# Kernel tuning notes

Measured on AMD Instinct MI355X. Metric: run time of the kernel, lower is better.

The kernel has to match this reference:

```python
import jax, jax.numpy as jnp
import numpy as np

N_G, N_D = 100000, 50000
E_GG, E_DG = 1600000, 800000
IN, HID, H, OUT = 128, 128, 8, 2
D = HID // H  # 16


def setup_inputs() -> dict:
    key = jax.random.key(0)
    ks = jax.random.split(key, 14)
    w = lambda k, s: jax.random.normal(k, s, dtype=jnp.float32) * 0.05
    return {
        "x_gene": jax.random.normal(ks[0], (N_G, IN), dtype=jnp.float32),
        "x_disease": jax.random.normal(ks[1], (N_D, IN), dtype=jnp.float32),
        "edge_gg": jax.random.randint(ks[2], (2, E_GG), 0, N_G),   # gene -> gene
        "edge_dg": jax.random.randint(ks[3], (2, E_DG), 0, N_D),   # disease -> gene (dst < N_D <= N_G)
        "proj_gene_w": w(ks[4], (HID, IN)),
        "proj_gene_b": jnp.zeros((HID,), jnp.float32),
        "proj_disease_w": w(ks[5], (HID, IN)),
        "proj_disease_b": jnp.zeros((HID,), jnp.float32),
        "att_src_gg": w(ks[6], (H, D)),
        "att_dst_gg": w(ks[7], (H, D)),
        "att_src_dg": w(ks[8], (H, D)),
        "att_dst_dg": w(ks[9], (H, D)),
        "k_lin_w": w(ks[10], (HID, HID)),
        "k_lin_b": jnp.zeros((HID,), jnp.float32),
        "q": w(ks[11], (HID,)),
        "lin_w": w(ks[12], (OUT, HID)),
        "lin_b": jnp.zeros((OUT,), jnp.float32),
    }


def _edge_type_out(x_src, x_dst, att_src, att_dst, src, dst, num_dst):
    """GAT-style message passing for one edge type. x_*: [N,H,D]."""
    a_s = (x_src * att_src).sum(-1)          # [Ns, H]
    a_d = (x_dst * att_dst).sum(-1)          # [Nd, H]
    a = a_s[src] + a_d[dst]                  # [E, H]
    a = jnp.where(a > 0, a, 0.2 * a)         # leaky_relu(0.2)
    # segment softmax over edges grouped by dst node
    m = jax.ops.segment_max(a, dst, num_segments=num_dst)
    m = jnp.where(jnp.isfinite(m), m, 0.0)
    e = jnp.exp(a - m[dst])
    s = jax.ops.segment_sum(e, dst, num_segments=num_dst)
    alpha = e / (s[dst] + 1e-16)             # [E, H]
    msg = x_src[src] * alpha[:, :, None]     # [E, H, D]
    out = jax.ops.segment_sum(msg, dst, num_segments=num_dst)
    return jax.nn.relu(out.reshape(num_dst, H * D))


def reference(x_gene, x_disease, edge_gg, edge_dg,
              proj_gene_w, proj_gene_b, proj_disease_w, proj_disease_b,
              att_src_gg, att_dst_gg, att_src_dg, att_dst_dg,
              k_lin_w, k_lin_b, q, lin_w, lin_b):
    # per-node-type projection, split into heads
    xg = (x_gene @ proj_gene_w.T + proj_gene_b).reshape(N_G, H, D)
    xd = (x_disease @ proj_disease_w.T + proj_disease_b).reshape(N_D, H, D)

    # node-level attention per edge type (dropout p=0.6 is train-only; eval mode here)
    out_gg = _edge_type_out(xg, xg, att_src_gg, att_dst_gg, edge_gg[0], edge_gg[1], N_G)
    out_dg = _edge_type_out(xd, xg, att_src_dg, att_dst_dg, edge_dg[0], edge_dg[1], N_G)

    # semantic-level attention across metapaths for dst type 'gene'
    outs = jnp.stack([out_gg, out_dg])                  # [2, N_G, HID]
    k = jnp.tanh(outs @ k_lin_w.T + k_lin_b)            # [2, N_G, HID]
    score = (q * k.mean(axis=1)).sum(-1)                # [2]
    attn = jax.nn.softmax(score, axis=0)
    fused = (attn[:, None, None] * outs).sum(0)         # [N_G, HID]

    return fused @ lin_w.T + lin_b                      # [N_G, OUT]
```

## Files before the change

### kernel.cpp

```cpp
#include <hip/hip_runtime.h>
#include <hip/hip_fp16.h>
#include <math.h>

#define NG 100000
#define ND 50000
#define EGG 1600000
#define EDG 800000
#define EALL (EGG + EDG)
#define NALL (NG + NG)
#define HID 128
#define NH 8

#define SHIFT 11
#define BDSTS (1 << SHIFT)
#define NBUK  ((NALL + BDSTS - 1) / BDSTS)
#define BUKCAP 36864
#define S1_CH 6144
#define KM_HALF ((NG + 127) / 128)

#define OFF_OUT_GG 0UL
#define OFF_OUT_DG 6400000UL
#define OFF_XG     12800000UL
#define OFF_XD     19200000UL
#define OFF_ASG    22400000UL
#define OFF_ADG    23200000UL
#define OFF_ADD    24000000UL
#define OFF_ASD    24800000UL
#define OFF_KPART  25200000UL
#define OFF_BCNT   25200256UL
#define ZERO_BASE  OFF_KPART
#define ZERO_CNT   384
#define OFF_ATTN   25200384UL
#define OFF_BBASE  25200512UL
#define OFF_RP     25200640UL
#define OFF_COL    25400704UL
#define OFF_WTIL   27800704UL
#define OFF_BTIL   27803776UL
#define OFF_WTILD  27803904UL
#define OFF_BTILD  27804928UL

typedef float  f32x4  __attribute__((ext_vector_type(4)));
typedef short  bf16x8 __attribute__((ext_vector_type(8)));
typedef _Float16 f16x8 __attribute__((ext_vector_type(8)));
#define MFMA(a, b, c)  __builtin_amdgcn_mfma_f32_16x16x32_bf16(a, b, c, 0, 0, 0)
#define MFMAH(a, b, c) __builtin_amdgcn_mfma_f32_16x16x32_f16(a, b, c, 0, 0, 0)

#define FMAMIX_LO(ACC, SRC, AL) \
    asm("v_fma_mix_f32 %0, %1, %2, %0 op_sel:[0,0,0] op_sel_hi:[1,0,0]" \
        : "+v"(ACC) : "v"(SRC), "v"(AL))
#define FMAMIX_HI(ACC, SRC, AL) \
    asm("v_fma_mix_f32 %0, %1, %2, %0 op_sel:[1,0,0] op_sel_hi:[1,0,0]" \
        : "+v"(ACC) : "v"(SRC), "v"(AL))

__device__ __forceinline__ unsigned short bf16_rne(float f) {
    unsigned u = __float_as_uint(f);
    u += 0x7FFFu + ((u >> 16) & 1u);
    return (unsigned short)(u >> 16);
}
__device__ __forceinline__ float bf16f(unsigned short h) {
    return __uint_as_float(((unsigned)h) << 16);
}
__device__ __forceinline__ unsigned short f16_bits(float f) {
    __half h = __float2half(f);
    return *(unsigned short*)&h;
}
__device__ __forceinline__ float fast_tanh(float x) {
    x = fminf(fmaxf(x, -15.f), 15.f);
    float t = __expf(2.f * x);
    return (t - 1.f) / (t + 1.f);
}
__device__ __forceinline__ bf16x8 cvt_hi8(f32x4 v0, f32x4 v1) {
    bf16x8 f;
    f[0] = (short)bf16_rne(v0.x); f[1] = (short)bf16_rne(v0.y);
    f[2] = (short)bf16_rne(v0.z); f[3] = (short)bf16_rne(v0.w);
    f[4] = (short)bf16_rne(v1.x); f[5] = (short)bf16_rne(v1.y);
    f[6] = (short)bf16_rne(v1.z); f[7] = (short)bf16_rne(v1.w);
    return f;
}
__device__ __forceinline__ bf16x8 cvt_lo8(f32x4 v0, f32x4 v1, bf16x8 h) {
    bf16x8 f;
    f[0] = (short)bf16_rne(v0.x - bf16f((unsigned short)h[0]));
    f[1] = (short)bf16_rne(v0.y - bf16f((unsigned short)h[1]));
    f[2] = (short)bf16_rne(v0.z - bf16f((unsigned short)h[2]));
    f[3] = (short)bf16_rne(v0.w - bf16f((unsigned short)h[3]));
    f[4] = (short)bf16_rne(v1.x - bf16f((unsigned short)h[4]));
    f[5] = (short)bf16_rne(v1.y - bf16f((unsigned short)h[5]));
    f[6] = (short)bf16_rne(v1.z - bf16f((unsigned short)h[6]));
    f[7] = (short)bf16_rne(v1.w - bf16f((unsigned short)h[7]));
    return f;
}
__device__ __forceinline__ unsigned relu_pk(unsigned u) {
    return u & ~(((u & 0x80008000u) >> 15) * 0xFFFFu);
}
union U4F16 { uint4 u; f16x8 f; };

__global__ void init_zero_k(float* __restrict__ p, int n) {
    int i = blockIdx.x * 256 + threadIdx.x;
    if (i < n) p[i] = 0.f;
}

__global__ void make_wtil(const float* __restrict__ W, const float* __restrict__ bias,
                          const float* __restrict__ a0, const float* __restrict__ a1,
                          const float* __restrict__ a2, int natt,
                          float* __restrict__ wtil, float* __restrict__ btil) {
    int tot = natt * 8 * 128;
    for (int i = blockIdx.x * 256 + threadIdx.x; i < tot; i += gridDim.x * 256) {
        int k = i & 127, cc = i >> 7;
        int v = cc >> 3, h = cc & 7;
        const float* av = (v == 0) ? a0 : (v == 1) ? a1 : a2;
        float s = 0.f;
        #pragma unroll
        for (int c = 0; c < 16; c++) s += av[h * 16 + c] * W[(h * 16 + c) * 128 + k];
        wtil[i] = s;
    }
    if (blockIdx.x == 0 && threadIdx.x < natt * 8) {
        int v = threadIdx.x >> 3, h = threadIdx.x & 7;
        const float* av = (v == 0) ? a0 : (v == 1) ? a1 : a2;
        float s = 0.f;
        #pragma unroll
        for (int c = 0; c < 16; c++) s += av[h * 16 + c] * bias[h * 16 + c];
        btil[threadIdx.x] = s;
    }
}

template<int NATT>
__launch_bounds__(256)
__global__ void proj_mfma(const float* __restrict__ x, const float* __restrict__ W,
                          const float* __restrict__ bias,
                          const float* __restrict__ wtil, const float* __restrict__ btil,
                          unsigned short* __restrict__ xbf,
                          float* __restrict__ o0, float* __restrict__ o1,
                          float* __restrict__ o2, int N) {
    constexpr int NTE = (NATT * 8 + 15) / 16;
    constexpr int NT = 8 + NTE;
    __shared__ bf16x8 Bhi[NT * 4 * 64];
    __shared__ bf16x8 Blo[8 * 4 * 64];
    for (int idx = threadIdx.x; idx < 128 * 32; idx += 256) {
        int row = idx >> 5, kq = idx & 31;
        f32x4 v = *(const f32x4*)&W[row * 128 + kq * 4];
        int ct = row >> 4, c = row & 15;
        int k0 = kq * 4;
        int kc = k0 >> 5, q16 = (k0 & 31) >> 3, j2 = (k0 & 7) >> 1;
        int slot = (ct * 4 + kc) * 64 + q16 * 16 + c;
        unsigned short hx = bf16_rne(v.x), hy = bf16_rne(v.y);
        unsigned short hz = bf16_rne(v.z), hw = bf16_rne(v.w);
        unsigned* dh = (unsigned*)&Bhi[slot];
        dh[j2]     = ((unsigned)hy << 16) | hx;
        dh[j2 + 1] = ((unsigned)hw << 16) | hz;
        unsigned* dl = (unsigned*)&Blo[slot];
        dl[j2]     = ((unsigned)bf16_rne(v.y - bf16f(hy)) << 16) | bf16_rne(v.x - bf16f(hx));
        dl[j2 + 1] = ((unsigned)bf16_rne(v.w - bf16f(hw)) << 16) | bf16_rne(v.z - bf16f(hz));
    }
    for (int idx = threadIdx.x; idx < NTE * 16 * 32; idx += 256) {
        int cc = idx >> 5, kq = idx & 31;
        f32x4 v = {0.f, 0.f, 0.f, 0.f};
        if (cc < NATT * 8) v = *(const f32x4*)&wtil[cc * 128 + kq * 4];
        int ct = 8 + (cc >> 4), c = cc & 15;
        int k0 = kq * 4;
        int kc = k0 >> 5, q16 = (k0 & 31) >> 3, j2 = (k0 & 7) >> 1;
        unsigned* dh = (unsigned*)&Bhi[(ct * 4 + kc) * 64 + q16 * 16 + c];
        dh[j2]     = ((unsigned)bf16_rne(v.y) << 16) | bf16_rne(v.x);
        dh[j2 + 1] = ((unsigned)bf16_rne(v.w) << 16) | bf16_rne(v.z);
    }
    __syncthreads();
    int wv = threadIdx.x >> 6, l = threadIdx.x & 63;
    int q = l >> 4, c16 = l & 15;
    int rw = blockIdx.x * 128 + wv * 32;
    int n0 = min(rw + c16, N - 1);
    int n1 = min(rw + 16 + c16, N - 1);
    const float* xr0 = &x[(size_t)n0 * 128 + q * 8];
    const float* xr1 = &x[(size_t)n1 * 128 + q * 8];
    #define LOADX(FH, FL, PTR, OFF) \
        bf16x8 FH, FL; \
        { f32x4 v0_ = *(const f32x4*)((PTR) + (OFF)); \
          f32x4 v1_ = *(const f32x4*)((PTR) + (OFF) + 4); \
          FH = cvt_hi8(v0_, v1_); FL = cvt_lo8(v0_, v1_, FH); }
    LOADX(xh00, xl00, xr0, 0)  LOADX(xh01, xl01, xr0, 32)
    LOADX(xh02, xl02, xr0, 64) LOADX(xh03, xl03, xr0, 96)
    LOADX(xh10, xl10, xr1, 0)  LOADX(xh11, xl11, xr1, 32)
    LOADX(xh12, xl12, xr1, 64) LOADX(xh13, xl13, xr1, 96)
    #undef LOADX
    int r0 = rw + q * 4;
    int r1 = r0 + 16;
    #define CT_MAIN(CT) { \
        bf16x8 bh0 = Bhi[((CT) * 4 + 0) * 64 + l]; \
        bf16x8 bh1 = Bhi[((CT) * 4 + 1) * 64 + l]; \
        bf16x8 bh2 = Bhi[((CT) * 4 + 2) * 64 + l]; \
        bf16x8 bh3 = Bhi[((CT) * 4 + 3) * 64 + l]; \
        bf16x8 bl0 = Blo[((CT) * 4 + 0) * 64 + l]; \
        bf16x8 bl1 = Blo[((CT) * 4 + 1) * 64 + l]; \
        bf16x8 bl2 = Blo[((CT) * 4 + 2) * 64 + l]; \
        bf16x8 bl3 = Blo[((CT) * 4 + 3) * 64 + l]; \
        f32x4 aA = {0,0,0,0}, aB = {0,0,0,0}, aC = {0,0,0,0}, aD = {0,0,0,0}; \
        aA = MFMA(xh00, bh0, aA); aB = MFMA(xh01, bh1, aB); \
        aC = MFMA(xh10, bh0, aC); aD = MFMA(xh11, bh1, aD); \
        aA = MFMA(xl00, bh0, aA); aB = MFMA(xl01, bh1, aB); \
        aC = MFMA(xl10, bh0, aC); aD = MFMA(xl11, bh1, aD); \
        aA = MFMA(xh00, bl0, aA); aB = MFMA(xh01, bl1, aB); \
        aC = MFMA(xh10, bl0, aC); aD = MFMA(xh11, bl1, aD); \
        aA = MFMA(xh02, bh2, aA); aB = MFMA(xh03, bh3, aB); \
        aC = MFMA(xh12, bh2, aC); aD = MFMA(xh13, bh3, aD); \
        aA = MFMA(xl02, bh2, aA); aB = MFMA(xl03, bh3, aB); \
        aC = MFMA(xl12, bh2, aC); aD = MFMA(xl13, bh3, aD); \
        aA = MFMA(xh02, bl2, aA); aB = MFMA(xh03, bl3, aB); \
        aC = MFMA(xh12, bl2, aC); aD = MFMA(xh13, bl3, aD); \
        f32x4 d0 = aA + aB, d1 = aC + aD; \
        float bv = bias[(CT) * 16 + c16]; \
        int col = (CT) * 16 + c16; \
        if (r0 + 0 < N) xbf[(size_t)(r0 + 0) * 128 + col] = f16_bits(d0[0] + bv); \
        if (r0 + 1 < N) xbf[(size_t)(r0 + 1) * 128 + col] = f16_bits(d0[1] + bv); \
        if (r0 + 2 < N) xbf[(size_t)(r0 + 2) * 128 + col] = f16_bits(d0[2] + bv); \
        if (r0 + 3 < N) xbf[(size_t)(r0 + 3) * 128 + col] = f16_bits(d0[3] + bv); \
        if (r1 + 0 < N) xbf[(size_t)(r1 + 0) * 128 + col] = f16_bits(d1[0] + bv); \
        if (r1 + 1 < N) xbf[(size_t)(r1 + 1) * 128 + col] = f16_bits(d1[1] + bv); \
        if (r1 + 2 < N) xbf[(size_t)(r1 + 2) * 128 + col] = f16_bits(d1[2] + bv); \
        if (r1 + 3 < N) xbf[(size_t)(r1 + 3) * 128 + col] = f16_bits(d1[3] + bv); }
    CT_MAIN(0) CT_MAIN(1) CT_MAIN(2) CT_MAIN(3)
    CT_MAIN(4) CT_MAIN(5) CT_MAIN(6) CT_MAIN(7)
    #undef CT_MAIN
    #define CT_ATT(TE) { \
        bf16x8 bh0 = Bhi[((8 + (TE)) * 4 + 0) * 64 + l]; \
        bf16x8 bh1 = Bhi[((8 + (TE)) * 4 + 1) * 64 + l]; \
        bf16x8 bh2 = Bhi[((8 + (TE)) * 4 + 2) * 64 + l]; \
        bf16x8 bh3 = Bhi[((8 + (TE)) * 4 + 3) * 64 + l]; \
        f32x4 aA = {0,0,0,0}, aB = {0,0,0,0}, aC = {0,0,0,0}, aD = {0,0,0,0}; \
        aA = MFMA(xh00, bh0, aA); aB = MFMA(xh01, bh1, aB); \
        aC = MFMA(xh10, bh0, aC); aD = MFMA(xh11, bh1, aD); \
        aA = MFMA(xh02, bh2, aA); aB = MFMA(xh03, bh3, aB); \
        aC = MFMA(xh12, bh2, aC); aD = MFMA(xh13, bh3, aD); \
        f32x4 d0 = aA + aB, d1 = aC + aD; \
        int cc = (TE) * 16 + c16; \
        if (cc < NATT * 8) { \
            float bt = btil[cc]; \
            int v = cc >> 3, h = cc & 7; \
            float* op = (v == 0) ? o0 : ((v == 1) ? o1 : o2); \
            if (r0 + 0 < N) op[(r0 + 0) * 8 + h] = d0[0] + bt; \
            if (r0 + 1 < N) op[(r0 + 1) * 8 + h] = d0[1] + bt; \
            if (r0 + 2 < N) op[(r0 + 2) * 8 + h] = d0[2] + bt; \
            if (r0 + 3 < N) op[(r0 + 3) * 8 + h] = d0[3] + bt; \
            if (r1 + 0 < N) op[(r1 + 0) * 8 + h] = d1[0] + bt; \
            if (r1 + 1 < N) op[(r1 + 1) * 8 + h] = d1[1] + bt; \
            if (r1 + 2 < N) op[(r1 + 2) * 8 + h] = d1[2] + bt; \
            if (r1 + 3 < N) op[(r1 + 3) * 8 + h] = d1[3] + bt; } }
    CT_ATT(0)
    if constexpr (NTE > 1) { CT_ATT(1) }
    #undef CT_ATT
}

__launch_bounds__(256)
__global__ void fused_scatter(const int* __restrict__ gg_src, const int* __restrict__ gg_dst,
                              const int* __restrict__ dg_src, const int* __restrict__ dg_dst,
                              int* __restrict__ bcnt, unsigned int* __restrict__ colPacked) {
    __shared__ int cnt[256], scanE[256], gbase[256], cursor[256];
    __shared__ int ss[256];
    __shared__ unsigned int sorted[S1_CH];
    __shared__ unsigned char bof[S1_CH];
    int t = threadIdx.x;
    cnt[t] = 0;
    __syncthreads();
    int base = blockIdx.x * S1_CH;
    for (int k = 0; k < S1_CH; k += 256) {
        int e = base + k + t;
        if (e < EALL) {
            int dn = (e < EGG) ? gg_dst[e] : (NG + dg_dst[e - EGG]);
            atomicAdd(&cnt[dn >> SHIFT], 1);
        }
    }
    __syncthreads();
    int v = cnt[t];
    ss[t] = v;
    __syncthreads();
    for (int off = 1; off < 256; off <<= 1) {
        int y = (t >= off) ? ss[t - off] : 0;
        __syncthreads();
        ss[t] += y;
        __syncthreads();
    }
    scanE[t] = ss[t] - v;
    cursor[t] = ss[t] - v;
    if (t < NBUK && v > 0) gbase[t] = atomicAdd(&bcnt[t], v);
    __syncthreads();
    for (int k = 0; k < S1_CH; k += 256) {
        int e = base + k + t;
        if (e < EALL) {
            int s, dn;
            if (e < EGG) { s = gg_src[e]; dn = gg_dst[e]; }
            else         { s = dg_src[e - EGG]; dn = NG + dg_dst[e - EGG]; }
            int b = dn >> SHIFT;
            int slot = atomicAdd(&cursor[b], 1);
            sorted[slot] = ((unsigned int)s << SHIFT) | (unsigned int)(dn & (BDSTS - 1));
            bof[slot] = (unsigned char)b;
        }
    }
    __syncthreads();
    int total = ss[255];
    for (int f = t; f < total; f += 256) {
        int b = bof[f];
        colPacked[(size_t)b * BUKCAP + gbase[b] + (f - scanE[b])] = sorted[f];
    }
}

__global__ void scan_buckets(const int* __restrict__ bcnt, int* __restrict__ bbase,
                             int* __restrict__ rp) {
    __shared__ int s[128];
    int t = threadIdx.x;
    int v = (t < NBUK) ? bcnt[t] : 0;
    s[t] = v;
    __syncthreads();
    for (int off = 1; off < 128; off <<= 1) {
        int y = (t >= off) ? s[t - off] : 0;
        __syncthreads();
        s[t] += y;
        __syncthreads();
    }
    if (t < NBUK) bbase[t] = s[t] - v;
    if (t == 0) rp[NALL] = EALL;
}

__launch_bounds__(256)
__global__ void bucket_build(const unsigned int* __restrict__ colPacked,
                             const int* __restrict__ bcnt, const int* __restrict__ bbase,
                             int* __restrict__ rp, int* __restrict__ col) {
    __shared__ int lcur[BDSTS];
    __shared__ int tsum[256];
    int b = blockIdx.x;
    int t = threadIdx.x;
    int d0 = b << SHIFT;
    int nd = min(BDSTS, NALL - d0);
    int cnt = bcnt[b];
    const unsigned int* pk = colPacked + (size_t)b * BUKCAP;
    for (int i = t; i < BDSTS; i += 256) lcur[i] = 0;
    __syncthreads();
    for (int i = t; i < cnt; i += 256)
        atomicAdd(&lcur[pk[i] & (BDSTS - 1)], 1);
    __syncthreads();
    int h0 = lcur[t * 8 + 0], h1 = lcur[t * 8 + 1], h2 = lcur[t * 8 + 2], h3 = lcur[t * 8 + 3];
    int h4 = lcur[t * 8 + 4], h5 = lcur[t * 8 + 5], h6 = lcur[t * 8 + 6], h7 = lcur[t * 8 + 7];
    int tot = h0 + h1 + h2 + h3 + h4 + h5 + h6 + h7;
    tsum[t] = tot;
    __syncthreads();
    for (int off = 1; off < 256; off <<= 1) {
        int y = (t >= off) ? tsum[t - off] : 0;
        __syncthreads();
        tsum[t] += y;
        __syncthreads();
    }
    int gb = bbase[b];
    int pp = tsum[t] - tot + gb;
    __syncthreads();
    #define EMIT(J, HJ) { int idx = t * 8 + (J); \
        if (idx < nd) rp[d0 + idx] = pp; \
        lcur[idx] = pp; pp += (HJ); }
    EMIT(0, h0) EMIT(1, h1) EMIT(2, h2) EMIT(3, h3)
    EMIT(4, h4) EMIT(5, h5) EMIT(6, h6) EMIT(7, h7)
    #undef EMIT
    __syncthreads();
    for (int i = t; i < cnt; i += 256) {
        unsigned int p = pk[i];
        int pos = atomicAdd(&lcur[p & (BDSTS - 1)], 1);
        col[pos] = (int)(p >> SHIFT);
    }
}

__launch_bounds__(256)
__global__ void gat_gather_all(const int* __restrict__ rp, const int* __restrict__ col,
                               const float* __restrict__ as_gg, const float* __restrict__ ad_gg,
                               const unsigned short* __restrict__ xg_h,
                               const float* __restrict__ as_dg, const float* __restrict__ ad_dg,
                               const unsigned short* __restrict__ xd_h,
                               unsigned short* __restrict__ out_gg,
                               unsigned short* __restrict__ out_dg) {
    int wid = (blockIdx.x * 256 + threadIdx.x) >> 6;
    int l = threadIdx.x & 63;
    if (wid >= NALL) return;
    int isdg = wid >= NG;
    int d = isdg ? wid - NG : wid;
    const float* a_s = isdg ? as_dg : as_gg;
    const float* a_d = isdg ? ad_dg : ad_gg;
    const unsigned short* xbf = isdg ? xd_h : xg_h;
    unsigned short* outh = (isdg ? out_dg : out_gg);

    int base = rp[wid];
    int deg = rp[wid + 1] - base;

    int hl = l & 7;
    int g  = l >> 3;
    float adl = a_d[d * 8 + hl];
    float ssum = 0.f;
    for (int c0 = 0; c0 < deg; c0 += 64) {
        int myi = c0 + l;
        int colreg = (myi < deg) ? col[base + myi] : 0;
        int lim = min(deg - c0, 64);
        for (int t = g; t < lim; t += 8) {
            int s = __shfl(colreg, t);
            float a = a_s[s * 8 + hl] + adl;
            a = a > 0.f ? a : 0.2f * a;
            ssum += __expf(a);
        }
    }
    ssum += __shfl_xor(ssum, 8);
    ssum += __shfl_xor(ssum, 16);
    ssum += __shfl_xor(ssum, 32);
    float rsc = 1.f / (ssum + 1e-16f);

    int q = l >> 4;
    int cq = l & 15;
    int hq = cq >> 1;
    uint32_t colbyte = (uint32_t)cq << 4;
    float a0 = 0.f, a1 = 0.f, a2 = 0.f, a3 = 0.f, a4 = 0.f, a5 = 0.f, a6 = 0.f, a7 = 0.f;
    for (int c0 = 0; c0 < deg; c0 += 64) {
        int myi = c0 + l;
        int colreg = (myi < deg) ? col[base + myi] : 0;
        int lim = min(deg - c0, 64);
        for (int j8 = 0; j8 < lim; j8 += 8) {
            float alpha;
            {
                int s = __shfl(colreg, j8 + g);
                float a = a_s[s * 8 + hl] + adl;
                a = a > 0.f ? a : 0.2f * a;
                alpha = __expf(a) * rsc;
            }
            int jlim = min(lim - j8, 8);
            #pragma unroll
            for (int sub = 0; sub < 8; sub += 4) {
                int jrel = sub + q;
                int s = __shfl(colreg, j8 + jrel);
                float al = __shfl(alpha, (jrel << 3) + hq);
                al = (jrel < jlim) ? al : 0.f;
                const uint4 rv = *(const uint4*)((const char*)xbf +
                                    (((size_t)(uint32_t)s << 8) + colbyte));
                FMAMIX_LO(a0, rv.x, al); FMAMIX_HI(a1, rv.x, al);
                FMAMIX_LO(a2, rv.y, al); FMAMIX_HI(a3, rv.y, al);
                FMAMIX_LO(a4, rv.z, al); FMAMIX_HI(a5, rv.z, al);
                FMAMIX_LO(a6, rv.w, al); FMAMIX_HI(a7, rv.w, al);
            }
        }
    }
    a0 += __shfl_xor(a0, 16); a0 += __shfl_xor(a0, 32);
    a1 += __shfl_xor(a1, 16); a1 += __shfl_xor(a1, 32);
    a2 += __shfl_xor(a2, 16); a2 += __shfl_xor(a2, 32);
    a3 += __shfl_xor(a3, 16); a3 += __shfl_xor(a3, 32);
    a4 += __shfl_xor(a4, 16); a4 += __shfl_xor(a4, 32);
    a5 += __shfl_xor(a5, 16); a5 += __shfl_xor(a5, 32);
    a6 += __shfl_xor(a6, 16); a6 += __shfl_xor(a6, 32);
    a7 += __shfl_xor(a7, 16); a7 += __shfl_xor(a7, 32);
    if (q == 0) {
        __half2 h01 = __floats2half2_rn(a0, a1);
        __half2 h23 = __floats2half2_rn(a2, a3);
        __half2 h45 = __floats2half2_rn(a4, a5);
        __half2 h67 = __floats2half2_rn(a6, a7);
        uint4 o;
        o.x = *(unsigned*)&h01; o.y = *(unsigned*)&h23;
        o.z = *(unsigned*)&h45; o.w = *(unsigned*)&h67;
        *(uint4*)((char*)outh + (size_t)d * 256 + cq * 16) = o;
    }
}

__launch_bounds__(256)
__global__ void kmean_mfma(const unsigned short* __restrict__ srcA,
                           const unsigned short* __restrict__ srcB,
                           const float* __restrict__ W, const float* __restrict__ bias,
                           float* __restrict__ kp) {
    __shared__ f16x8 Bs[8 * 4 * 64];
    for (int idx = threadIdx.x; idx < 128 * 32; idx += 256) {
        int row = idx >> 5, kq = idx & 31;
        f32x4 v = *(const f32x4*)&W[row * 128 + kq * 4];
        int ct = row >> 4, c = row & 15;
        int k0 = kq * 4;
        int kc = k0 >> 5, q16 = (k0 & 31) >> 3, j2 = (k0 & 7) >> 1;
        unsigned* dst = (unsigned*)&Bs[(ct * 4 + kc) * 64 + q16 * 16 + c];
        dst[j2]     = ((unsigned)f16_bits(v.y) << 16) | f16_bits(v.x);
        dst[j2 + 1] = ((unsigned)f16_bits(v.w) << 16) | f16_bits(v.z);
    }
    __syncthreads();
    int half = blockIdx.x >= KM_HALF;
    const unsigned short* src = half ? srcB : srcA;
    float* kpp = half ? (kp + 128) : kp;
    int rb = (half ? blockIdx.x - KM_HALF : blockIdx.x) * 128;
    int wv = threadIdx.x >> 6, l = threadIdx.x & 63;
    int q = l >> 4, c16 = l & 15;
    int rw = rb + wv * 32;
    const char* xr0 = (const char*)src + (size_t)(rw + c16) * 256 + q * 16;
    const char* xr1 = xr0 + 16 * 256;
    #define LOADA(F, PTR, OFF) f16x8 F; { \
        U4F16 u_; u_.u = *(const uint4*)((PTR) + (OFF)); \
        u_.u.x = relu_pk(u_.u.x); u_.u.y = relu_pk(u_.u.y); \
        u_.u.z = relu_pk(u_.u.z); u_.u.w = relu_pk(u_.u.w); \
        F = u_.f; }
    LOADA(f00, xr0, 0) LOADA(f01, xr0, 64) LOADA(f02, xr0, 128) LOADA(f03, xr0, 192)
    LOADA(f10, xr1, 0) LOADA(f11, xr1, 64) LOADA(f12, xr1, 128) LOADA(f13, xr1, 192)
    #undef LOADA
    float bv0 = bias[c16],      bv1 = bias[16 + c16], bv2 = bias[32 + c16], bv3 = bias[48 + c16];
    float bv4 = bias[64 + c16], bv5 = bias[80 + c16], bv6 = bias[96 + c16], bv7 = bias[112 + c16];
    int row0 = rw + q * 4;
    int row1 = row0 + 16;
    float cs0 = 0.f, cs1 = 0.f, cs2 = 0.f, cs3 = 0.f, cs4 = 0.f, cs5 = 0.f, cs6 = 0.f, cs7 = 0.f;
    #define CT_STEP(CT, CS, BV) { \
        f16x8 b0 = Bs[((CT) * 4 + 0) * 64 + l]; \
        f16x8 b1 = Bs[((CT) * 4 + 1) * 64 + l]; \
        f16x8 b2 = Bs[((CT) * 4 + 2) * 64 + l]; \
        f16x8 b3 = Bs[((CT) * 4 + 3) * 64 + l]; \
        f32x4 aA = {0,0,0,0}, aB = {0,0,0,0}, aC = {0,0,0,0}, aD = {0,0,0,0}; \
        aA = MFMAH(f00, b0, aA); aB = MFMAH(f01, b1, aB); \
        aA = MFMAH(f02, b2, aA); aB = MFMAH(f03, b3, aB); \
        aC = MFMAH(f10, b0, aC); aD = MFMAH(f11, b1, aD); \
        aC = MFMAH(f12, b2, aC); aD = MFMAH(f13, b3, aD); \
        f32x4 d0 = aA + aB, d1 = aC + aD; \
        float s = 0.f; \
        if (row0 + 0 < NG) s += fast_tanh(d0[0] + (BV)); \
        if (row0 + 1 < NG) s += fast_tanh(d0[1] + (BV)); \
        if (row0 + 2 < NG) s += fast_tanh(d0[2] + (BV)); \
        if (row0 + 3 < NG) s += fast_tanh(d0[3] + (BV)); \
        if (row1 + 0 < NG) s += fast_tanh(d1[0] + (BV)); \
        if (row1 + 1 < NG) s += fast_tanh(d1[1] + (BV)); \
        if (row1 + 2 < NG) s += fast_tanh(d1[2] + (BV)); \
        if (row1 + 3 < NG) s += fast_tanh(d1[3] + (BV)); \
        CS += s; }
    CT_STEP(0, cs0, bv0) CT_STEP(1, cs1, bv1) CT_STEP(2, cs2, bv2) CT_STEP(3, cs3, bv3)
    CT_STEP(4, cs4, bv4) CT_STEP(5, cs5, bv5) CT_STEP(6, cs6, bv6) CT_STEP(7, cs7, bv7)
    #undef CT_STEP
    __syncthreads();
    float* red = (float*)Bs;
    #define REDUCE_CT(CT, CS) { \
        float v = (CS); \
        v += __shfl_xor(v, 16); v += __shfl_xor(v, 32); \
        if (l < 16) red[wv * 128 + (CT) * 16 + l] = v; }
    REDUCE_CT(0, cs0) REDUCE_CT(1, cs1) REDUCE_CT(2, cs2) REDUCE_CT(3, cs3)
    REDUCE_CT(4, cs4) REDUCE_CT(5, cs5) REDUCE_CT(6, cs6) REDUCE_CT(7, cs7)
    #undef REDUCE_CT
    __syncthreads();
    if (threadIdx.x < 128) {
        float s = red[threadIdx.x] + red[128 + threadIdx.x]
                + red[256 + threadIdx.x] + red[384 + threadIdx.x];
        atomicAdd(&kpp[threadIdx.x], s);
    }
}

__global__ void score_attn(const float* __restrict__ kpart, const float* __restrict__ q,
                           float* __restrict__ attn) {
    __shared__ float r0[128], r1[128];
    int t = threadIdx.x;
    r0[t] = q[t] * kpart[t];
    r1[t] = q[t] * kpart[128 + t];
    __syncthreads();
    for (int s = 64; s > 0; s >>= 1) {
        if (t < s) { r0[t] += r0[t + s]; r1[t] += r1[t + s]; }
        __syncthreads();
    }
    if (t == 0) {
        float s0 = r0[0] / (float)NG, s1 = r1[0] / (float)NG;
        float mx = fmaxf(s0, s1);
        float e0 = expf(s0 - mx), e1 = expf(s1 - mx);
        attn[0] = e0 / (e0 + e1);
        attn[1] = e1 / (e0 + e1);
    }
}

__launch_bounds__(256)
__global__ void final_lin(const unsigned short* __restrict__ gg,
                          const unsigned short* __restrict__ dgb,
                          const float* __restrict__ attn, const float* __restrict__ lin_w,
                          const float* __restrict__ lin_b, float* __restrict__ outp) {
    int wid = (blockIdx.x * 256 + threadIdx.x) >> 6;
    int l = threadIdx.x & 63;
    if (wid >= NG) return;
    float a0 = attn[0], a1 = attn[1];
    unsigned gu = *(const unsigned*)((const char*)gg + (size_t)wid * 256 + l * 4);
    unsigned du = *(const unsigned*)((const char*)dgb + (size_t)wid * 256 + l * 4);
    float2 gv = __half22float2(*(const __half2*)&gu);
    float2 dv = __half22float2(*(const __half2*)&du);
    float fx = a0 * fmaxf(gv.x, 0.f) + a1 * fmaxf(dv.x, 0.f);
    float fy = a0 * fmaxf(gv.y, 0.f) + a1 * fmaxf(dv.y, 0.f);
    float2 w0 = *(const float2*)&lin_w[l * 2];
    float2 w1 = *(const float2*)&lin_w[128 + l * 2];
    float p0 = fx * w0.x + fy * w0.y;
    float p1 = fx * w1.x + fy * w1.y;
    for (int off = 32; off > 0; off >>= 1) {
        p0 += __shfl_down(p0, off);
        p1 += __shfl_down(p1, off);
    }
    if (l == 0) {
        float2 o;
        o.x = p0 + lin_b[0];
        o.y = p1 + lin_b[1];
        *(float2*)&outp[wid * 2] = o;
    }
}

extern "C" void kernel_launch(void* const* d_in, const int* in_sizes, int n_in,
                              void* d_out, int out_size, void* d_ws, size_t ws_size,
                              hipStream_t stream) {
    const float* x_gene    = (const float*)d_in[0];
    const float* x_disease = (const float*)d_in[1];
    const int*   edge_gg   = (const int*)d_in[2];
    const int*   edge_dg   = (const int*)d_in[3];
    const float* pg_w      = (const float*)d_in[4];
    const float* pg_b      = (const float*)d_in[5];
    const float* pd_w      = (const float*)d_in[6];
    const float* pd_b      = (const float*)d_in[7];
    const float* att_src_gg= (const float*)d_in[8];
    const float* att_dst_gg= (const float*)d_in[9];
    const float* att_src_dg= (const float*)d_in[10];
    const float* att_dst_dg= (const float*)d_in[11];
    const float* k_lin_w   = (const float*)d_in[12];
    const float* k_lin_b   = (const float*)d_in[13];
    const float* q         = (const float*)d_in[14];
    const float* lin_w     = (const float*)d_in[15];
    const float* lin_b     = (const float*)d_in[16];
    float* out = (float*)d_out;
    float* ws  = (float*)d_ws;

    unsigned short* out_gg = (unsigned short*)(ws + OFF_OUT_GG);
    unsigned short* out_dg = (unsigned short*)(ws + OFF_OUT_DG);
    unsigned int* colPacked = (unsigned int*)(ws + OFF_OUT_GG);
    unsigned short* xg_h = (unsigned short*)(ws + OFF_XG);
    unsigned short* xd_h = (unsigned short*)(ws + OFF_XD);
    float* a_src_gg = ws + OFF_ASG;
    float* a_dst_gg = ws + OFF_ADG;
    float* a_dst_dg = ws + OFF_ADD;
    float* a_src_dg = ws + OFF_ASD;
    float* kpart  = ws + OFF_KPART;
    float* attn   = ws + OFF_ATTN;
    float* wtilG  = ws + OFF_WTIL;
    float* btilG  = ws + OFF_BTIL;
    float* wtilD  = ws + OFF_WTILD;
    float* btilD  = ws + OFF_BTILD;
    int* bcnt  = (int*)(ws + OFF_BCNT);
    int* bbase = (int*)(ws + OFF_BBASE);
    int* rp    = (int*)(ws + OFF_RP);
    int* col   = (int*)(ws + OFF_COL);

    const int* gg_src = edge_gg;
    const int* gg_dst = edge_gg + EGG;
    const int* dg_src = edge_dg;
    const int* dg_dst = edge_dg + EDG;

    hipLaunchKernelGGL(init_zero_k, dim3(2), dim3(256), 0, stream, ws + ZERO_BASE, ZERO_CNT);
    hipLaunchKernelGGL(make_wtil, dim3(8), dim3(256), 0, stream,
                       pg_w, pg_b, att_src_gg, att_dst_gg, att_dst_dg, 3, wtilG, btilG);
    hipLaunchKernelGGL(make_wtil, dim3(4), dim3(256), 0, stream,
                       pd_w, pd_b, att_src_dg, att_src_dg, att_src_dg, 1, wtilD, btilD);
    hipLaunchKernelGGL((proj_mfma<3>), dim3((NG + 127) / 128), dim3(256), 0, stream,
                       x_gene, pg_w, pg_b, wtilG, btilG, xg_h,
                       a_src_gg, a_dst_gg, a_dst_dg, NG);
    hipLaunchKernelGGL((proj_mfma<1>), dim3((ND + 127) / 128), dim3(256), 0, stream,
                       x_disease, pd_w, pd_b, wtilD, btilD, xd_h,
                       a_src_dg, (float*)nullptr, (float*)nullptr, ND);
    hipLaunchKernelGGL(fused_scatter, dim3((EALL + S1_CH - 1) / S1_CH), dim3(256), 0, stream,
                       gg_src, gg_dst, dg_src, dg_dst, bcnt, colPacked);
    hipLaunchKernelGGL(scan_buckets, dim3(1), dim3(128), 0, stream, bcnt, bbase, rp);
    hipLaunchKernelGGL(bucket_build, dim3(NBUK), dim3(256), 0, stream,
                       colPacked, bcnt, bbase, rp, col);
    hipLaunchKernelGGL(gat_gather_all, dim3((NALL + 3) / 4), dim3(256), 0, stream,
                       rp, col, a_src_gg, a_dst_gg, xg_h, a_src_dg, a_dst_dg, xd_h,
                       out_gg, out_dg);
    hipLaunchKernelGGL(kmean_mfma, dim3(KM_HALF * 2), dim3(256), 0, stream,
                       out_gg, out_dg, k_lin_w, k_lin_b, kpart);
    hipLaunchKernelGGL(score_attn, dim3(1), dim3(128), 0, stream, kpart, q, attn);
    hipLaunchKernelGGL(final_lin, dim3((NG + 3) / 4), dim3(256), 0, stream,
                       out_gg, out_dg, attn, lin_w, lin_b, out);
}
```

Before: 374.8 us.

## Merge small setup kernels and simplify GAT gather to recompute alpha per lane

```diff
diff --git a/kernel.cpp b/kernel.cpp
--- a/kernel.cpp
+++ b/kernel.cpp
@@ -31,7 +31,6 @@
 #define ZERO_BASE  OFF_KPART
 #define ZERO_CNT   384
 #define OFF_ATTN   25200384UL
-#define OFF_BBASE  25200512UL
 #define OFF_RP     25200640UL
 #define OFF_COL    25400704UL
 #define OFF_WTIL   27800704UL
@@ -99,12 +98,15 @@
     if (i < n) p[i] = 0.f;
 }
 
-__global__ void make_wtil(const float* __restrict__ W, const float* __restrict__ bias,
-                          const float* __restrict__ a0, const float* __restrict__ a1,
-                          const float* __restrict__ a2, int natt,
-                          float* __restrict__ wtil, float* __restrict__ btil) {
+__device__ __forceinline__ void wtil_body(const float* __restrict__ W,
+                                          const float* __restrict__ bias,
+                                          const float* __restrict__ a0,
+                                          const float* __restrict__ a1,
+                                          const float* __restrict__ a2, int natt,
+                                          float* __restrict__ wtil, float* __restrict__ btil,
+                                          int bid, int nblk) {
     int tot = natt * 8 * 128;
-    for (int i = blockIdx.x * 256 + threadIdx.x; i < tot; i += gridDim.x * 256) {
+    for (int i = bid * 256 + threadIdx.x; i < tot; i += nblk * 256) {
         int k = i & 127, cc = i >> 7;
         int v = cc >> 3, h = cc & 7;
         const float* av = (v == 0) ? a0 : (v == 1) ? a1 : a2;
@@ -113,7 +115,7 @@
         for (int c = 0; c < 16; c++) s += av[h * 16 + c] * W[(h * 16 + c) * 128 + k];
         wtil[i] = s;
     }
-    if (blockIdx.x == 0 && threadIdx.x < natt * 8) {
+    if (bid == 0 && threadIdx.x < natt * 8) {
         int v = threadIdx.x >> 3, h = threadIdx.x & 7;
         const float* av = (v == 0) ? a0 : (v == 1) ? a1 : a2;
         float s = 0.f;
@@ -121,6 +123,19 @@
         for (int c = 0; c < 16; c++) s += av[h * 16 + c] * bias[h * 16 + c];
         btil[threadIdx.x] = s;
     }
+}
+
+__global__ void make_wtil_both(const float* __restrict__ Wg, const float* __restrict__ bg,
+                               const float* __restrict__ ag0, const float* __restrict__ ag1,
+                               const float* __restrict__ ag2,
+                               const float* __restrict__ Wd, const float* __restrict__ bd,
+                               const float* __restrict__ ad0,
+                               float* __restrict__ wtilG, float* __restrict__ btilG,
+                               float* __restrict__ wtilD, float* __restrict__ btilD) {
+    if (blockIdx.x < 8)
+        wtil_body(Wg, bg, ag0, ag1, ag2, 3, wtilG, btilG, blockIdx.x, 8);
+    else
+        wtil_body(Wd, bd, ad0, ad0, ad0, 1, wtilD, btilD, blockIdx.x - 8, 4);
 }
 
 template<int NATT>
@@ -300,31 +315,25 @@
     }
 }
 
-__global__ void scan_buckets(const int* __restrict__ bcnt, int* __restrict__ bbase,
-                             int* __restrict__ rp) {
-    __shared__ int s[128];
-    int t = threadIdx.x;
-    int v = (t < NBUK) ? bcnt[t] : 0;
-    s[t] = v;
-    __syncthreads();
-    for (int off = 1; off < 128; off <<= 1) {
-        int y = (t >= off) ? s[t - off] : 0;
-        __syncthreads();
-        s[t] += y;
-        __syncthreads();
-    }
-    if (t < NBUK) bbase[t] = s[t] - v;
-    if (t == 0) rp[NALL] = EALL;
-}
-
 __launch_bounds__(256)
 __global__ void bucket_build(const unsigned int* __restrict__ colPacked,
-                             const int* __restrict__ bcnt, const int* __restrict__ bbase,
+                             const int* __restrict__ bcnt,
                              int* __restrict__ rp, int* __restrict__ col) {
     __shared__ int lcur[BDSTS];
     __shared__ int tsum[256];
+    __shared__ int bscan[128];
     int b = blockIdx.x;
     int t = threadIdx.x;
+    if (t < 128) bscan[t] = (t < NBUK) ? bcnt[t] : 0;
+    __syncthreads();
+    for (int off = 1; off < 128; off <<= 1) {
+        int y = 0;
+        if (t < 128 && t >= off) y = bscan[t - off];
+        __syncthreads();
+        if (t < 128) bscan[t] += y;
+        __syncthreads();
+    }
+    int gb = (b > 0) ? bscan[b - 1] : 0;
     int d0 = b << SHIFT;
     int nd = min(BDSTS, NALL - d0);
     int cnt = bcnt[b];
@@ -345,7 +354,6 @@
         tsum[t] += y;
         __syncthreads();
     }
-    int gb = bbase[b];
     int pp = tsum[t] - tot + gb;
     __syncthreads();
     #define EMIT(J, HJ) { int idx = t * 8 + (J); \
@@ -354,6 +362,7 @@
     EMIT(0, h0) EMIT(1, h1) EMIT(2, h2) EMIT(3, h3)
     EMIT(4, h4) EMIT(5, h5) EMIT(6, h6) EMIT(7, h7)
     #undef EMIT
+    if (b == NBUK - 1 && t == 0) rp[NALL] = EALL;
     __syncthreads();
     for (int i = t; i < cnt; i += 256) {
         unsigned int p = pk[i];
@@ -387,16 +396,11 @@
     int g  = l >> 3;
     float adl = a_d[d * 8 + hl];
     float ssum = 0.f;
-    for (int c0 = 0; c0 < deg; c0 += 64) {
-        int myi = c0 + l;
-        int colreg = (myi < deg) ? col[base + myi] : 0;
-        int lim = min(deg - c0, 64);
-        for (int t = g; t < lim; t += 8) {
-            int s = __shfl(colreg, t);
-            float a = a_s[s * 8 + hl] + adl;
-            a = a > 0.f ? a : 0.2f * a;
-            ssum += __expf(a);
-        }
+    for (int t = g; t < deg; t += 8) {
+        int s = col[base + t];
+        float a = a_s[s * 8 + hl] + adl;
+        a = a > 0.f ? a : 0.2f * a;
+        ssum += __expf(a);
     }
     ssum += __shfl_xor(ssum, 8);
     ssum += __shfl_xor(ssum, 16);
@@ -406,36 +410,29 @@
     int q = l >> 4;
     int cq = l & 15;
     int hq = cq >> 1;
+    float rscq = __shfl(rsc, hq);
+    float adq = a_d[d * 8 + hq];
     uint32_t colbyte = (uint32_t)cq << 4;
     float a0 = 0.f, a1 = 0.f, a2 = 0.f, a3 = 0.f, a4 = 0.f, a5 = 0.f, a6 = 0.f, a7 = 0.f;
-    for (int c0 = 0; c0 < deg; c0 += 64) {
-        int myi = c0 + l;
-        int colreg = (myi < deg) ? col[base + myi] : 0;
-        int lim = min(deg - c0, 64);
-        for (int j8 = 0; j8 < lim; j8 += 8) {
-            float alpha;
-            {
-                int s = __shfl(colreg, j8 + g);
-                float a = a_s[s * 8 + hl] + adl;
-                a = a > 0.f ? a : 0.2f * a;
-                alpha = __expf(a) * rsc;
-            }
-            int jlim = min(lim - j8, 8);
-            #pragma unroll
-            for (int sub = 0; sub < 8; sub += 4) {
-                int jrel = sub + q;
-                int s = __shfl(colreg, j8 + jrel);
-                float al = __shfl(alpha, (jrel << 3) + hq);
-                al = (jrel < jlim) ? al : 0.f;
-                const uint4 rv = *(const uint4*)((const char*)xbf +
-                                    (((size_t)(uint32_t)s << 8) + colbyte));
-                FMAMIX_LO(a0, rv.x, al); FMAMIX_HI(a1, rv.x, al);
-                FMAMIX_LO(a2, rv.y, al); FMAMIX_HI(a3, rv.y, al);
-                FMAMIX_LO(a4, rv.z, al); FMAMIX_HI(a5, rv.z, al);
-                FMAMIX_LO(a6, rv.w, al); FMAMIX_HI(a7, rv.w, al);
-            }
+    for (int j = 0; j < deg; j += 8) {
+        #pragma unroll
+        for (int sub = 0; sub < 8; sub += 4) {
+            int jrel = j + sub + q;
+            bool ok = jrel < deg;
+            int s = ok ? col[base + jrel] : 0;
+            float a = a_s[s * 8 + hq] + adq;
+            a = a > 0.f ? a : 0.2f * a;
+            float al = ok ? __expf(a) : 0.f;
+            const uint4 rv = *(const uint4*)((const char*)xbf +
+                                (((size_t)(uint32_t)s << 8) + colbyte));
+            FMAMIX_LO(a0, rv.x, al); FMAMIX_HI(a1, rv.x, al);
+            FMAMIX_LO(a2, rv.y, al); FMAMIX_HI(a3, rv.y, al);
+            FMAMIX_LO(a4, rv.z, al); FMAMIX_HI(a5, rv.z, al);
+            FMAMIX_LO(a6, rv.w, al); FMAMIX_HI(a7, rv.w, al);
         }
     }
+    a0 *= rscq; a1 *= rscq; a2 *= rscq; a3 *= rscq;
+    a4 *= rscq; a5 *= rscq; a6 *= rscq; a7 *= rscq;
     a0 += __shfl_xor(a0, 16); a0 += __shfl_xor(a0, 32);
     a1 += __shfl_xor(a1, 16); a1 += __shfl_xor(a1, 32);
     a2 += __shfl_xor(a2, 16); a2 += __shfl_xor(a2, 32);
@@ -626,7 +623,6 @@
     float* wtilD  = ws + OFF_WTILD;
     float* btilD  = ws + OFF_BTILD;
     int* bcnt  = (int*)(ws + OFF_BCNT);
-    int* bbase = (int*)(ws + OFF_BBASE);
     int* rp    = (int*)(ws + OFF_RP);
     int* col   = (int*)(ws + OFF_COL);
 
@@ -636,10 +632,9 @@
     const int* dg_dst = edge_dg + EDG;
 
     hipLaunchKernelGGL(init_zero_k, dim3(2), dim3(256), 0, stream, ws + ZERO_BASE, ZERO_CNT);
-    hipLaunchKernelGGL(make_wtil, dim3(8), dim3(256), 0, stream,
-                       pg_w, pg_b, att_src_gg, att_dst_gg, att_dst_dg, 3, wtilG, btilG);
-    hipLaunchKernelGGL(make_wtil, dim3(4), dim3(256), 0, stream,
-                       pd_w, pd_b, att_src_dg, att_src_dg, att_src_dg, 1, wtilD, btilD);
+    hipLaunchKernelGGL(make_wtil_both, dim3(12), dim3(256), 0, stream,
+                       pg_w, pg_b, att_src_gg, att_dst_gg, att_dst_dg,
+                       pd_w, pd_b, att_src_dg, wtilG, btilG, wtilD, btilD);
     hipLaunchKernelGGL((proj_mfma<3>), dim3((NG + 127) / 128), dim3(256), 0, stream,
                        x_gene, pg_w, pg_b, wtilG, btilG, xg_h,
                        a_src_gg, a_dst_gg, a_dst_dg, NG);
@@ -648,9 +643,8 @@
                        a_src_dg, (float*)nullptr, (float*)nullptr, ND);
     hipLaunchKernelGGL(fused_scatter, dim3((EALL + S1_CH - 1) / S1_CH), dim3(256), 0, stream,
                        gg_src, gg_dst, dg_src, dg_dst, bcnt, colPacked);
-    hipLaunchKernelGGL(scan_buckets, dim3(1), dim3(128), 0, stream, bcnt, bbase, rp);
     hipLaunchKernelGGL(bucket_build, dim3(NBUK), dim3(256), 0, stream,
-                       colPacked, bcnt, bbase, rp, col);
+                       colPacked, bcnt, rp, col);
     hipLaunchKernelGGL(gat_gather_all, dim3((NALL + 3) / 4), dim3(256), 0, stream,
                        rp, col, a_src_gg, a_dst_gg, xg_h, a_src_dg, a_dst_dg, xd_h,
                        out_gg, out_dg);
```

Result: slower. 419.5 us (+11.9%).
